# Performance work log

Measured on AMD Instinct MI355X. Metric: run time of the kernel, lower is better.

Reference implementation:

```python
import jax, jax.numpy as jnp
import numpy as np
import math

B, S, E, H = 2, 4096, 1024, 1024

def setup_inputs() -> dict:
    key = jax.random.key(0)
    ks = jax.random.split(key, 7)
    X = jax.random.normal(ks[0], (B, S, E), dtype=jnp.float32)
    attention_mask = jnp.ones((B, S, S), dtype=jnp.int32)
    sc = 1.0 / math.sqrt(E)
    Wq = jax.random.normal(ks[1], (H, E), dtype=jnp.float32) * sc
    Wk = jax.random.normal(ks[2], (H, E), dtype=jnp.float32) * sc
    Wv = jax.random.normal(ks[3], (H, E), dtype=jnp.float32) * sc
    bq = jnp.zeros((H,), dtype=jnp.float32)
    bk = jnp.zeros((H,), dtype=jnp.float32)
    bv = jnp.zeros((H,), dtype=jnp.float32)
    return {"X": X, "attention_mask": attention_mask,
            "Wq": Wq, "bq": bq, "Wk": Wk, "bk": bk, "Wv": Wv, "bv": bv}

def reference(X, attention_mask, Wq, bq, Wk, bk, Wv, bv):
    # Linear layers: y = x @ W^T + b (torch convention W is [out, in])
    Q = jnp.einsum('bse,he->bsh', X, Wq) + bq
    K = jnp.einsum('bse,he->bsh', X, Wk) + bk
    V = jnp.einsum('bse,he->bsh', X, Wv) + bv
    scale = 1.0 / math.sqrt(H)
    scores = jnp.einsum('bqh,bkh->bqk', Q, K) * scale  # [B,S,S]
    scores = jnp.where(attention_mask == 0, -jnp.inf, scores)
    # dropout (eval mode -> identity) would be applied here, BEFORE softmax
    weights = jax.nn.softmax(scores, axis=-1)
    out = jnp.einsum('bqk,bkh->bqh', weights, V)  # [B,S,H]
    return out
```

## Files before the change

kernel.cpp:

```cpp
#include <hip/hip_runtime.h>
#include <stdint.h>


typedef __bf16 bf16;
typedef __attribute__((ext_vector_type(4))) __bf16 bf16x4;
typedef __attribute__((ext_vector_type(8))) __bf16 bf16x8;
typedef __attribute__((ext_vector_type(4))) float f32x4;

__device__ __forceinline__ void g2l16(const void* g, void* l) {
  __builtin_amdgcn_global_load_lds(
      (const __attribute__((address_space(1))) uint32_t*)g,
      (__attribute__((address_space(3))) uint32_t*)l, 16, 0, 0);
}

__device__ __forceinline__ f32x4 ds_read128(uint32_t addr) {
  f32x4 d;
  asm volatile("ds_read_b128 %0, %1" : "=v"(d) : "v"(addr));
  return d;
}

template <int V> struct IC { static constexpr int value = V; };
template <bool V> struct BC { static constexpr bool value = V; };

template <int N> __device__ __forceinline__ void waitvm() {
  if constexpr (N == 6) asm volatile("s_waitcnt vmcnt(6)" ::: "memory");
  else if constexpr (N == 4) asm volatile("s_waitcnt vmcnt(4)" ::: "memory");
  else if constexpr (N == 0) asm volatile("s_waitcnt vmcnt(0)" ::: "memory");
}

__global__ __launch_bounds__(256) void cvt_f32_bf16(
    const float* __restrict__ src, bf16* __restrict__ dst, int n) {
  const int i = (blockIdx.x * 256 + threadIdx.x) * 8;
  if (i >= n) return;
  f32x4 a = *(const f32x4*)(src + i);
  f32x4 b = *(const f32x4*)(src + i + 4);
  bf16x8 o;
#pragma unroll
  for (int e = 0; e < 4; ++e) { o[e] = (bf16)a[e]; o[4 + e] = (bf16)b[e]; }
  *(bf16x8*)(dst + i) = o;
}

__global__ __launch_bounds__(256) void cvt_w3(
    const float* __restrict__ Wq, const float* __restrict__ Wk,
    const float* __restrict__ Wv, bf16* __restrict__ dst) {
  const int i = (blockIdx.x * 256 + threadIdx.x) * 8;
  const int seg = i >> 20;
  const int off = i & 1048575;
  const float* src = (seg == 0) ? Wq : (seg == 1) ? Wk : Wv;
  f32x4 a = *(const f32x4*)(src + off);
  f32x4 b = *(const f32x4*)(src + off + 4);
  bf16x8 o;
#pragma unroll
  for (int e = 0; e < 4; ++e) { o[e] = (bf16)a[e]; o[4 + e] = (bf16)b[e]; }
  *(bf16x8*)(dst + i) = o;
}

template <int NT>
__device__ __forceinline__ void kloop256(
    const bf16* __restrict__ Ag, const bf16* __restrict__ Bg, const int KA,
    const int KB, bf16* lds, f32x4 (&acc)[8][4]) {
  const int tid = threadIdx.x;
  const int lane = tid & 63;
  const int wave = tid >> 6;
  const int l15 = lane & 15, quad = lane >> 4;
  const int wrow = (wave >> 2) * 128;
  const int wcol = (wave & 3) * 64;
  const int srow = tid >> 3;
  const int scol = ((tid & 7) ^ (srow & 7)) * 8;
  const int swz = l15 & 7;

  const uint32_t lds_u = (uint32_t)(uintptr_t)lds;
  const uint32_t a_l15 = lds_u + (uint32_t)((wrow + l15) * 128);
  const uint32_t b_l15 = lds_u + 32768u + (uint32_t)((wcol + l15) * 128);
  const uint32_t ck0 = (uint32_t)(((quad) ^ swz) * 16);
  const uint32_t ck1 = (uint32_t)(((4 + quad) ^ swz) * 16);

  auto stg = [&](int t, int h) {
    bf16* base = lds + (t & 1) * 32768;
    if (h == 0) {
      const bf16* g = Bg + (size_t)srow * KB + t * 64 + scol;
      g2l16(g, base + 16384 + tid * 8);
      g2l16(g + (size_t)64 * KB, base + 16384 + tid * 8 + 4096);
    } else if (h == 1) {
      const bf16* g = Bg + (size_t)(128 + srow) * KB + t * 64 + scol;
      g2l16(g, base + 24576 + tid * 8);
      g2l16(g + (size_t)64 * KB, base + 24576 + tid * 8 + 4096);
    } else if (h == 2) {
      const bf16* g = Ag + (size_t)srow * KA + t * 64 + scol;
      g2l16(g, base + tid * 8);
      g2l16(g + (size_t)128 * KA, base + tid * 8 + 8192);
    } else {
      const bf16* g = Ag + (size_t)(64 + srow) * KA + t * 64 + scol;
      g2l16(g, base + 4096 + tid * 8);
      g2l16(g + (size_t)128 * KA, base + 4096 + tid * 8 + 8192);
    }
  };

  f32x4 brf[2][4];
  auto phase = [&](int t, auto qc, int st, int sh, auto dsc, auto vmc) {
    constexpr int q = decltype(qc)::value;
    constexpr bool ds = decltype(dsc)::value;
    constexpr int vm = decltype(vmc)::value;
    const uint32_t bb = (t & 1) ? 65536u : 0u;
    f32x4 ar[2][2];
#pragma unroll
    for (int i = 0; i < 2; ++i) {
      ar[i][0] = ds_read128(a_l15 + bb + (uint32_t)((2 * q + i) * 2048) + ck0);
      ar[i][1] = ds_read128(a_l15 + bb + (uint32_t)((2 * q + i) * 2048) + ck1);
    }
    if constexpr (q == 0) {
#pragma unroll
      for (int j = 0; j < 4; ++j) {
        brf[0][j] = ds_read128(b_l15 + bb + (uint32_t)(j * 2048) + ck0);
        brf[1][j] = ds_read128(b_l15 + bb + (uint32_t)(j * 2048) + ck1);
      }
    }
    if constexpr (ds) stg(st, sh);
    __builtin_amdgcn_s_barrier();
    asm volatile("s_waitcnt lgkmcnt(0)" ::: "memory");
    __builtin_amdgcn_sched_barrier(0);
    __builtin_amdgcn_s_setprio(1);
#pragma unroll
    for (int ks = 0; ks < 2; ++ks)
#pragma unroll
      for (int i = 0; i < 2; ++i)
#pragma unroll
        for (int j = 0; j < 4; ++j)
          acc[2 * q + i][j] = __builtin_amdgcn_mfma_f32_16x16x32_bf16(
              __builtin_bit_cast(bf16x8, ar[i][ks]),
              __builtin_bit_cast(bf16x8, brf[ks][j]),
              acc[2 * q + i][j], 0, 0, 0);
    __builtin_amdgcn_s_setprio(0);
    waitvm<vm>();
    __builtin_amdgcn_s_barrier();
  };

  stg(0, 0); stg(0, 1); stg(0, 2); stg(0, 3);
  stg(1, 0); stg(1, 1); stg(1, 2);
  asm volatile("s_waitcnt vmcnt(6)" ::: "memory");
  __builtin_amdgcn_s_barrier();

  constexpr int NI = NT / 2;
#pragma unroll 1
  for (int u = 0; u < NI - 1; ++u) {
    const int t0 = 2 * u, t1 = t0 + 1;
    phase(t0, IC<0>{}, t1, 3, BC<true>{}, IC<-1>{});
    phase(t0, IC<1>{}, t0 + 2, 0, BC<true>{}, IC<-1>{});
    phase(t0, IC<2>{}, t0 + 2, 1, BC<true>{}, IC<-1>{});
    phase(t0, IC<3>{}, t0 + 2, 2, BC<true>{}, IC<6>{});
    phase(t1, IC<0>{}, t0 + 2, 3, BC<true>{}, IC<-1>{});
    phase(t1, IC<1>{}, t0 + 3, 0, BC<true>{}, IC<-1>{});
    phase(t1, IC<2>{}, t0 + 3, 1, BC<true>{}, IC<-1>{});
    phase(t1, IC<3>{}, t0 + 3, 2, BC<true>{}, IC<6>{});
  }
  {
    const int t0 = NT - 2, t1 = NT - 1;
    phase(t0, IC<0>{}, t1, 3, BC<true>{}, IC<-1>{});
    phase(t0, IC<1>{}, 0, 0, BC<false>{}, IC<-1>{});
    phase(t0, IC<2>{}, 0, 0, BC<false>{}, IC<-1>{});
    phase(t0, IC<3>{}, 0, 0, BC<false>{}, IC<0>{});
    phase(t1, IC<0>{}, 0, 0, BC<false>{}, IC<-1>{});
    phase(t1, IC<1>{}, 0, 0, BC<false>{}, IC<-1>{});
    phase(t1, IC<2>{}, 0, 0, BC<false>{}, IC<-1>{});
    phase(t1, IC<3>{}, 0, 0, BC<false>{}, IC<-1>{});
  }
}

__global__ __launch_bounds__(256, 4) void gemm_qkv(
    const bf16* __restrict__ Xb, const bf16* __restrict__ Wb3,
    const float* __restrict__ bq, const float* __restrict__ bk,
    const float* __restrict__ bv, bf16* __restrict__ QK,
    bf16* __restrict__ Vt)
{
  constexpr int K = 1024, N = 1024;
  __shared__ __align__(16) bf16 ldsA[128 * 64];
  __shared__ __align__(16) bf16 ldsB[128 * 64];

  const int tid  = threadIdx.x;
  const int lane = tid & 63;
  const int wave = tid >> 6;
  const int bid = blockIdx.y * 64 + blockIdx.x;
  const int sb = (bid & 7) * 192 + (bid >> 3);
  const int bx = sb & 63, by = sb >> 6;
  const int which = by >> 3;
  const int n0 = (by & 7) * 128;
  const int m0 = bx * 128;
  const bf16* Bt = Wb3 + (size_t)which * 1048576;
  const float* bias = (which == 0) ? bq : ((which == 1) ? bk : bv);

  const int l15  = lane & 15;
  const int quad = lane >> 4;
  const int wm = (wave >> 1) * 64;
  const int wn = (wave & 1) * 64;
  const int sw = l15 & 7;

  f32x4 acc[4][4];
#pragma unroll
  for (int i = 0; i < 4; ++i)
#pragma unroll
    for (int j = 0; j < 4; ++j) acc[i][j] = f32x4{0.f, 0.f, 0.f, 0.f};

  const int srow = tid >> 3;
  const int scol = ((tid & 7) ^ (srow & 7)) * 8;
  const size_t a_base = (size_t)(m0 + srow) * K + scol;
  const size_t b_base = (size_t)(n0 + srow) * K + scol;
  const int lds_off = tid * 8;

  for (int kt = 0; kt < K; kt += 64) {
    const bf16* ga = Xb + a_base + kt;
    const bf16* gb = Bt + b_base + kt;
#pragma unroll
    for (int it = 0; it < 4; ++it) {
      g2l16(ga + (size_t)(it * 32) * K, &ldsA[lds_off + it * 2048]);
      g2l16(gb + (size_t)(it * 32) * K, &ldsB[lds_off + it * 2048]);
    }
    __syncthreads();
#pragma unroll
    for (int ks = 0; ks < 2; ++ks) {
      const int ch = ks * 4 + quad;
      bf16x8 af[4], bfg[4];
#pragma unroll
      for (int i = 0; i < 4; ++i)
        af[i] = *(const bf16x8*)&ldsA[(wm + i * 16 + l15) * 64 + (ch ^ sw) * 8];
#pragma unroll
      for (int j = 0; j < 4; ++j)
        bfg[j] = *(const bf16x8*)&ldsB[(wn + j * 16 + l15) * 64 + (ch ^ sw) * 8];
#pragma unroll
      for (int i = 0; i < 4; ++i)
#pragma unroll
        for (int j = 0; j < 4; ++j)
          acc[i][j] = __builtin_amdgcn_mfma_f32_16x16x32_bf16(
              af[i], bfg[j], acc[i][j], 0, 0, 0);
    }
    __syncthreads();
  }

  if (which < 2) {
    bf16* C = QK + (size_t)which * (size_t)(8192 * 1024);
#pragma unroll
    for (int i = 0; i < 4; ++i) {
#pragma unroll
      for (int j = 0; j < 4; ++j) {
        const int r = m0 + wm + i * 16 + quad * 4;
        const int c = n0 + wn + j * 16 + l15;
        const float bvv = bias[c];
        f32x4 v = acc[i][j];
#pragma unroll
        for (int reg = 0; reg < 4; ++reg)
          C[(size_t)(r + reg) * N + c] = (bf16)(v[reg] + bvv);
      }
    }
  } else {
#pragma unroll
    for (int i = 0; i < 4; ++i) {
#pragma unroll
      for (int j = 0; j < 4; ++j) {
        const int r = m0 + wm + i * 16 + quad * 4;
        const int c = n0 + wn + j * 16 + l15;
        const int b = r >> 12, s = r & 4095;
        const float bvv = bias[c];
        f32x4 v = acc[i][j];
        bf16x4 o;
#pragma unroll
        for (int reg = 0; reg < 4; ++reg) o[reg] = (bf16)(v[reg] + bvv);
        *(bf16x4*)&Vt[((size_t)(b * 1024 + c)) * 4096 + s] = o;
      }
    }
  }
}

__global__ __launch_bounds__(512, 2) void gemm_scores(
    const bf16* __restrict__ Q, const bf16* __restrict__ Kb,
    const int* __restrict__ mask, bf16* __restrict__ P,
    float* __restrict__ row_sum) {
  __shared__ __align__(16) bf16 lds[2 * 32768];
  const int bid = blockIdx.y * 32 + blockIdx.x;
  const int sb = (bid & 7) * 64 + (bid >> 3);
  const int bx = sb & 31, by = sb >> 5;
  const int m0 = bx * 256;
  const int n0 = by * 256;
  const int batch = m0 >> 12;
  const bf16* Ag = Q + (size_t)m0 * 1024;
  const bf16* Bg = Kb + (size_t)batch * (size_t)(4096 * 1024) +
                   (size_t)n0 * 1024;

  f32x4 acc[8][4];
#pragma unroll
  for (int i = 0; i < 8; ++i)
#pragma unroll
    for (int j = 0; j < 4; ++j) acc[i][j] = f32x4{0.f, 0.f, 0.f, 0.f};

  kloop256<16>(Ag, Bg, 1024, 1024, lds, acc);

  const int lane = threadIdx.x & 63, wave = threadIdx.x >> 6;
  const int l15 = lane & 15, quad = lane >> 4;
  const int wrow = (wave >> 2) * 128, wcol = (wave & 3) * 64;

#pragma unroll
  for (int i = 0; i < 8; ++i) {
    const int r = m0 + wrow + i * 16 + quad * 4;
    f32x4 rsum = f32x4{0.f, 0.f, 0.f, 0.f};
#pragma unroll
    for (int j = 0; j < 4; ++j) {
      const int c = n0 + wcol + j * 16 + l15;
      f32x4 v = acc[i][j];
#pragma unroll
      for (int reg = 0; reg < 4; ++reg) {
        float e = __expf(v[reg] * 0.03125f);
        if (mask[(size_t)(r + reg) * 4096 + c] == 0) e = 0.f;
        P[(size_t)(r + reg) * 4096 + c] = (bf16)e;
        rsum[reg] += e;
      }
    }
#pragma unroll
    for (int off = 1; off < 16; off <<= 1) {
#pragma unroll
      for (int reg = 0; reg < 4; ++reg)
        rsum[reg] += __shfl_xor(rsum[reg], off);
    }
    if (l15 == 0) {
#pragma unroll
      for (int reg = 0; reg < 4; ++reg)
        atomicAdd(&row_sum[r + reg], rsum[reg]);
    }
  }
}

__global__ __launch_bounds__(256, 4) void gemm_pv(
    const bf16* __restrict__ A, const bf16* __restrict__ Bt,
    const float* __restrict__ row_sum, float* __restrict__ C)
{
  constexpr int N = 1024, K = 4096;
  __shared__ __align__(16) bf16 ldsA[128 * 64];
  __shared__ __align__(16) bf16 ldsB[128 * 64];

  const int tid  = threadIdx.x;
  const int lane = tid & 63;
  const int wave = tid >> 6;
  const int bid = blockIdx.y * 64 + blockIdx.x;
  const int sb = (bid & 7) * 64 + (bid >> 3);
  const int bx = sb & 63, by = sb >> 6;
  const int m0 = bx * 128;
  const int n0 = by * 128;
  const int batch = m0 >> 12;
  const bf16* Btb = Bt + (size_t)batch * (size_t)(1024 * 4096);

  const int l15  = lane & 15;
  const int quad = lane >> 4;
  const int wm = (wave >> 1) * 64;
  const int wn = (wave & 1) * 64;
  const int sw = l15 & 7;

  f32x4 acc[4][4];
#pragma unroll
  for (int i = 0; i < 4; ++i)
#pragma unroll
    for (int j = 0; j < 4; ++j) acc[i][j] = f32x4{0.f, 0.f, 0.f, 0.f};

  const int srow = tid >> 3;
  const int scol = ((tid & 7) ^ (srow & 7)) * 8;
  const size_t a_base = (size_t)(m0 + srow) * K + scol;
  const size_t b_base = (size_t)(n0 + srow) * K + scol;
  const int lds_off = tid * 8;

  for (int kt = 0; kt < K; kt += 64) {
    const bf16* ga = A + a_base + kt;
    const bf16* gb = Btb + b_base + kt;
#pragma unroll
    for (int it = 0; it < 4; ++it) {
      g2l16(ga + (size_t)(it * 32) * K, &ldsA[lds_off + it * 2048]);
      g2l16(gb + (size_t)(it * 32) * K, &ldsB[lds_off + it * 2048]);
    }
    __syncthreads();
#pragma unroll
    for (int ks = 0; ks < 2; ++ks) {
      const int ch = ks * 4 + quad;
      bf16x8 af[4], bfg[4];
#pragma unroll
      for (int i = 0; i < 4; ++i)
        af[i] = *(const bf16x8*)&ldsA[(wm + i * 16 + l15) * 64 + (ch ^ sw) * 8];
#pragma unroll
      for (int j = 0; j < 4; ++j)
        bfg[j] = *(const bf16x8*)&ldsB[(wn + j * 16 + l15) * 64 + (ch ^ sw) * 8];
#pragma unroll
      for (int i = 0; i < 4; ++i)
#pragma unroll
        for (int j = 0; j < 4; ++j)
          acc[i][j] = __builtin_amdgcn_mfma_f32_16x16x32_bf16(
              af[i], bfg[j], acc[i][j], 0, 0, 0);
    }
    __syncthreads();
  }

#pragma unroll
  for (int i = 0; i < 4; ++i) {
    const int r = m0 + wm + i * 16 + quad * 4;
    f32x4 inv;
#pragma unroll
    for (int reg = 0; reg < 4; ++reg) inv[reg] = 1.0f / row_sum[r + reg];
#pragma unroll
    for (int j = 0; j < 4; ++j) {
      const int c = n0 + wn + j * 16 + l15;
      f32x4 v = acc[i][j];
#pragma unroll
      for (int reg = 0; reg < 4; ++reg)
        C[(size_t)(r + reg) * N + c] = v[reg] * inv[reg];
    }
  }
}

extern "C" void kernel_launch(void* const* d_in, const int* in_sizes, int n_in,
                              void* d_out, int out_size, void* d_ws,
                              size_t ws_size, hipStream_t stream) {
  const float* X   = (const float*)d_in[0];
  const int* mask  = (const int*)d_in[1];
  const float* Wq  = (const float*)d_in[2];
  const float* bq  = (const float*)d_in[3];
  const float* Wk  = (const float*)d_in[4];
  const float* bk  = (const float*)d_in[5];
  const float* Wv  = (const float*)d_in[6];
  const float* bv  = (const float*)d_in[7];
  float* out = (float*)d_out;

  const size_t QKV_ELEMS = (size_t)8192 * 1024;
  bf16* Q    = (bf16*)d_ws;
  bf16* Kb   = Q + QKV_ELEMS;
  bf16* X_bf = Kb + QKV_ELEMS;
  bf16* Vt   = X_bf + QKV_ELEMS;
  bf16* Sc   = Vt + QKV_ELEMS;
  bf16* W_bf = Sc;
  float* row_sum = (float*)X_bf;

  cvt_f32_bf16<<<dim3(4096), dim3(256), 0, stream>>>(X, X_bf, 8388608);
  cvt_w3<<<dim3(1536), dim3(256), 0, stream>>>(Wq, Wk, Wv, W_bf);
  gemm_qkv<<<dim3(64, 24), dim3(256), 0, stream>>>(X_bf, W_bf, bq, bk, bv, Q,
                                                   Vt);
  hipMemsetAsync(row_sum, 0, 8192 * sizeof(float), stream);
  gemm_scores<<<dim3(32, 16), dim3(512), 0, stream>>>(Q, Kb, mask, Sc,
                                                      row_sum);
  gemm_pv<<<dim3(64, 8), dim3(256), 0, stream>>>(Sc, Vt, row_sum, out);
}
```

Before: 517.7 us.

## Pack attention mask into bitmask and remap GEMM blocks per XCD

Adds a pre-pass that packs the int32 attention mask into 64-bit ballot bitmasks. The scores epilogue then reads one 64-bit word per row segment instead of one int per element, which cuts the scattered mask traffic in that kernel. The full 128MB mask is still read once by the pack kernel, and it now runs as a separate launch. It also remaps block indices in gemm_qkv and gemm_pv so each XCD gets contiguous M tiles, and lowers their launch-bounds occupancy hint from 4 to 2.

Result: faster. 456.3 us (-11.9%).

```diff
diff --git a/kernel.cpp b/kernel.cpp
--- a/kernel.cpp
+++ b/kernel.cpp
@@ -53,6 +53,19 @@
 #pragma unroll
   for (int e = 0; e < 4; ++e) { o[e] = (bf16)a[e]; o[4 + e] = (bf16)b[e]; }
   *(bf16x8*)(dst + i) = o;
+}
+
+__global__ __launch_bounds__(256) void pack_mask(
+    const int* __restrict__ m, unsigned long long* __restrict__ bm,
+    int n) {
+  const int gw = (blockIdx.x * 256 + threadIdx.x) >> 6;
+  const int lane = threadIdx.x & 63;
+  const int nw = (2048 * 256) >> 6;
+  for (int base = gw * 64; base < n; base += nw * 64) {
+    const int v = m[base + lane];
+    const unsigned long long b = __ballot(v != 0);
+    if (lane == 0) bm[base >> 6] = b;
+  }
 }
 
 template <int NT>
@@ -166,7 +179,7 @@
   }
 }
 
-__global__ __launch_bounds__(256, 4) void gemm_qkv(
+__global__ __launch_bounds__(256, 2) void gemm_qkv(
     const bf16* __restrict__ Xb, const bf16* __restrict__ Wb3,
     const float* __restrict__ bq, const float* __restrict__ bk,
     const float* __restrict__ bv, bf16* __restrict__ QK,
@@ -179,12 +192,13 @@
   const int tid  = threadIdx.x;
   const int lane = tid & 63;
   const int wave = tid >> 6;
-  const int bid = blockIdx.y * 64 + blockIdx.x;
-  const int sb = (bid & 7) * 192 + (bid >> 3);
-  const int bx = sb & 63, by = sb >> 6;
-  const int which = by >> 3;
-  const int n0 = (by & 7) * 128;
-  const int m0 = bx * 128;
+  const int d = blockIdx.y * 64 + blockIdx.x;
+  const int xcd = d & 7, slot = d >> 3;
+  const int g = xcd * 8 + slot / 24;
+  const int c = slot % 24;
+  const int which = c >> 3;
+  const int n0 = (c & 7) * 128;
+  const int m0 = g * 128;
   const bf16* Bt = Wb3 + (size_t)which * 1048576;
   const float* bias = (which == 0) ? bq : ((which == 1) ? bk : bv);
 
@@ -242,12 +256,12 @@
 #pragma unroll
       for (int j = 0; j < 4; ++j) {
         const int r = m0 + wm + i * 16 + quad * 4;
-        const int c = n0 + wn + j * 16 + l15;
-        const float bvv = bias[c];
+        const int cc = n0 + wn + j * 16 + l15;
+        const float bvv = bias[cc];
         f32x4 v = acc[i][j];
 #pragma unroll
         for (int reg = 0; reg < 4; ++reg)
-          C[(size_t)(r + reg) * N + c] = (bf16)(v[reg] + bvv);
+          C[(size_t)(r + reg) * N + cc] = (bf16)(v[reg] + bvv);
       }
     }
   } else {
@@ -256,14 +270,14 @@
 #pragma unroll
       for (int j = 0; j < 4; ++j) {
         const int r = m0 + wm + i * 16 + quad * 4;
-        const int c = n0 + wn + j * 16 + l15;
+        const int cc = n0 + wn + j * 16 + l15;
         const int b = r >> 12, s = r & 4095;
-        const float bvv = bias[c];
+        const float bvv = bias[cc];
         f32x4 v = acc[i][j];
         bf16x4 o;
 #pragma unroll
         for (int reg = 0; reg < 4; ++reg) o[reg] = (bf16)(v[reg] + bvv);
-        *(bf16x4*)&Vt[((size_t)(b * 1024 + c)) * 4096 + s] = o;
+        *(bf16x4*)&Vt[((size_t)(b * 1024 + cc)) * 4096 + s] = o;
       }
     }
   }
@@ -271,7 +285,7 @@
 
 __global__ __launch_bounds__(512, 2) void gemm_scores(
     const bf16* __restrict__ Q, const bf16* __restrict__ Kb,
-    const int* __restrict__ mask, bf16* __restrict__ P,
+    const unsigned long long* __restrict__ BM, bf16* __restrict__ P,
     float* __restrict__ row_sum) {
   __shared__ __align__(16) bf16 lds[2 * 32768];
   const int bid = blockIdx.y * 32 + blockIdx.x;
@@ -295,10 +309,15 @@
   const int lane = threadIdx.x & 63, wave = threadIdx.x >> 6;
   const int l15 = lane & 15, quad = lane >> 4;
   const int wrow = (wave >> 2) * 128, wcol = (wave & 3) * 64;
+  const int bmcol = (n0 + wcol) >> 6;
 
 #pragma unroll
   for (int i = 0; i < 8; ++i) {
     const int r = m0 + wrow + i * 16 + quad * 4;
+    unsigned long long mrow[4];
+#pragma unroll
+    for (int reg = 0; reg < 4; ++reg)
+      mrow[reg] = BM[(size_t)(r + reg) * 64 + bmcol];
     f32x4 rsum = f32x4{0.f, 0.f, 0.f, 0.f};
 #pragma unroll
     for (int j = 0; j < 4; ++j) {
@@ -307,7 +326,7 @@
 #pragma unroll
       for (int reg = 0; reg < 4; ++reg) {
         float e = __expf(v[reg] * 0.03125f);
-        if (mask[(size_t)(r + reg) * 4096 + c] == 0) e = 0.f;
+        if (((mrow[reg] >> (j * 16 + l15)) & 1ull) == 0) e = 0.f;
         P[(size_t)(r + reg) * 4096 + c] = (bf16)e;
         rsum[reg] += e;
       }
@@ -326,7 +345,7 @@
   }
 }
 
-__global__ __launch_bounds__(256, 4) void gemm_pv(
+__global__ __launch_bounds__(256, 2) void gemm_pv(
     const bf16* __restrict__ A, const bf16* __restrict__ Bt,
     const float* __restrict__ row_sum, float* __restrict__ C)
 {
@@ -337,11 +356,12 @@
   const int tid  = threadIdx.x;
   const int lane = tid & 63;
   const int wave = tid >> 6;
-  const int bid = blockIdx.y * 64 + blockIdx.x;
-  const int sb = (bid & 7) * 64 + (bid >> 3);
-  const int bx = sb & 63, by = sb >> 6;
-  const int m0 = bx * 128;
-  const int n0 = by * 128;
+  const int d = blockIdx.y * 64 + blockIdx.x;
+  const int xcd = d & 7, slot = d >> 3;
+  const int g = xcd * 8 + (slot >> 3);
+  const int h = slot & 7;
+  const int m0 = g * 128;
+  const int n0 = h * 128;
   const int batch = m0 >> 12;
   const bf16* Btb = Bt + (size_t)batch * (size_t)(1024 * 4096);
 
@@ -430,13 +450,16 @@
   bf16* Sc   = Vt + QKV_ELEMS;
   bf16* W_bf = Sc;
   float* row_sum = (float*)X_bf;
+  unsigned long long* BM =
+      (unsigned long long*)((char*)X_bf + 65536);
 
   cvt_f32_bf16<<<dim3(4096), dim3(256), 0, stream>>>(X, X_bf, 8388608);
   cvt_w3<<<dim3(1536), dim3(256), 0, stream>>>(Wq, Wk, Wv, W_bf);
   gemm_qkv<<<dim3(64, 24), dim3(256), 0, stream>>>(X_bf, W_bf, bq, bk, bv, Q,
                                                    Vt);
+  pack_mask<<<dim3(2048), dim3(256), 0, stream>>>(mask, BM, 33554432);
   hipMemsetAsync(row_sum, 0, 8192 * sizeof(float), stream);
-  gemm_scores<<<dim3(32, 16), dim3(512), 0, stream>>>(Q, Kb, mask, Sc,
+  gemm_scores<<<dim3(32, 16), dim3(512), 0, stream>>>(Q, Kb, BM, Sc,
                                                       row_sum);
   gemm_pv<<<dim3(64, 8), dim3(256), 0, stream>>>(Sc, Vt, row_sum, out);
 }
```
